# Kernel tuning notes

Measured on AMD Instinct MI355X. Metric: run time of the kernel, lower is better.

Reference implementation:

```python
import jax, jax.numpy as jnp
import numpy as np

EPS = 1e-12  # tf.math.l2_normalize epsilon

def _l2norm(x):
    # normalize over last axis, matching K.l2_normalize semantics
    sq = jnp.sum(x * x, axis=-1, keepdims=True)
    return x * jax.lax.rsqrt(jnp.maximum(sq, EPS))

def setup_inputs() -> dict:
    key = jax.random.key(0)
    k1, k2, k3 = jax.random.split(key, 3)
    B, L, D, P = 16, 256, 256, 20
    sent1 = jax.random.normal(k1, (B, L, D), dtype=jnp.float32)
    sent2 = jax.random.normal(k2, (B, L, D), dtype=jnp.float32)
    # glorot_uniform for shape (P, D)
    limit = np.sqrt(6.0 / (P + D)).astype(np.float32)
    kernel = jax.random.uniform(k3, (P, D), minval=-limit, maxval=limit, dtype=jnp.float32)
    return {"sent1": sent1, "sent2": sent2, "kernel": kernel}

def reference(sent1, sent2, kernel):
    # sent1: [B,L1,D], sent2: [B,L2,D], kernel: [P,D]
    v1 = _l2norm(sent1[:, :, None, :] * kernel)  # [B,L1,P,D]
    v2 = _l2norm(sent2[:, :, None, :] * kernel)  # [B,L2,P,D]
    # per-perspective cosine similarity matrix: [B,L1,L2,P]
    cos = jnp.einsum('blpd,bmpd->blmp', v1, v2)
    # max over the other sentence's positions (L2) -> [B,L1,P]
    return jnp.max(cos, axis=2)
```

## Files before the change

### kernel.cpp

```cpp
#include <hip/hip_runtime.h>
#include <hip/hip_bf16.h>


#define B_DIM 16
#define L_DIM 256
#define D_DIM 256
#define P_DIM 20
#define EPS 1e-12f
#define LDP 264

typedef __attribute__((ext_vector_type(8))) __bf16 bf16x8;
typedef __attribute__((ext_vector_type(4))) float f32x4;

__device__ __forceinline__ unsigned short f2bf(float x) {
  unsigned int u = __float_as_uint(x);
  u += 0x7fffu + ((u >> 16) & 1u);
  return (unsigned short)(u >> 16);
}

__global__ __launch_bounds__(256)
void prep2(const float* __restrict__ s1, const float* __restrict__ s2,
           const float* __restrict__ kg,
           float* __restrict__ rn1, float* __restrict__ rn2,
           unsigned short* __restrict__ s1bf, unsigned short* __restrict__ s2bf) {
  __shared__ __align__(16) unsigned short QA[32 * LDP];
  __shared__ __align__(16) unsigned short QB[32 * LDP];
  const int tid = threadIdx.x, lane = tid & 63, wave = tid >> 6;
  const int lr = lane & 15, q = lane >> 4;
  const int sent = blockIdx.x & 1, t = blockIdx.x >> 1;
  const int r0 = t * 32, b = r0 >> 8;
  const float* src = sent ? s2 : s1;
  unsigned short* sbf = sent ? s2bf : s1bf;
  float* rn = sent ? rn2 : rn1;

  #pragma unroll
  for (int i = 0; i < 8; ++i) {
    const int row = i * 4 + wave;
    float4 sv = *(const float4*)(src + (size_t)(r0 + row) * D_DIM + lane * 4);
    unsigned int c0 = ((unsigned int)f2bf(sv.y) << 16) | f2bf(sv.x);
    unsigned int c1 = ((unsigned int)f2bf(sv.w) << 16) | f2bf(sv.z);
    *(uint2*)&sbf[(size_t)(r0 + row) * D_DIM + lane * 4] = make_uint2(c0, c1);
    unsigned int q0 = ((unsigned int)f2bf(sv.y * sv.y) << 16) | f2bf(sv.x * sv.x);
    unsigned int q1 = ((unsigned int)f2bf(sv.w * sv.w) << 16) | f2bf(sv.z * sv.z);
    *(uint2*)&QA[row * LDP + lane * 4] = make_uint2(q0, q1);
  }
  #pragma unroll
  for (int j = 0; j < 5; ++j) {
    const int row = wave * 5 + j;
    float4 kv = *(const float4*)(kg + row * D_DIM + lane * 4);
    unsigned int c0 = ((unsigned int)f2bf(kv.y * kv.y) << 16) | f2bf(kv.x * kv.x);
    unsigned int c1 = ((unsigned int)f2bf(kv.w * kv.w) << 16) | f2bf(kv.z * kv.z);
    *(uint2*)&QB[row * LDP + lane * 4] = make_uint2(c0, c1);
  }
  __syncthreads();

  const int mt = wave & 1, nt = wave >> 1;
  f32x4 acc = {0.f, 0.f, 0.f, 0.f};
  #pragma unroll
  for (int ks = 0; ks < 8; ++ks) {
    const int cc = ks * 4 + q;
    bf16x8 a  = *(const bf16x8*)&QA[(mt * 16 + lr) * LDP + cc * 8];
    bf16x8 bb = *(const bf16x8*)&QB[(nt * 16 + lr) * LDP + cc * 8];
    acc = __builtin_amdgcn_mfma_f32_16x16x32_bf16(a, bb, acc, 0, 0, 0);
  }
  const int p = nt * 16 + lr;
  if (p < P_DIM) {
    #pragma unroll
    for (int r = 0; r < 4; ++r) {
      const int l = (r0 & 255) + mt * 16 + q * 4 + r;
      rn[((size_t)b * P_DIM + p) * L_DIM + l] = rsqrtf(fmaxf(acc[r], EPS));
    }
  }
}

__global__ __launch_bounds__(512, 4)
void mpm_main(const unsigned short* __restrict__ s1bf,
              const unsigned short* __restrict__ s2bf,
              const float* __restrict__ kg, const float* __restrict__ rn1,
              const float* __restrict__ rn2, float* __restrict__ outg) {
  __shared__ __align__(16) unsigned short X1[32 * 256];
  __shared__ float Wout[8 * 32];

  const int tid = threadIdx.x, lane = tid & 63, wave = tid >> 6;
  const int lr = lane & 15, q = lane >> 4;

  const int bid = (int)((blockIdx.x >> 3) + (blockIdx.x & 7) * 64);
  const int pgi = bid & 3, lt = (bid >> 2) & 7, b = bid >> 5;
  const int l0 = lt * 32;

  bf16x8 af[2][8];
  {
    const unsigned short* s2b2 = s2bf + (size_t)b * (L_DIM * D_DIM);
    #pragma unroll
    for (int mi = 0; mi < 2; ++mi) {
      const unsigned short* rp = s2b2 + (size_t)(wave * 32 + mi * 16 + lr) * D_DIM + q * 8;
      #pragma unroll
      for (int ks = 0; ks < 8; ++ks)
        af[mi][ks] = *(const bf16x8*)(rp + ks * 32);
    }
  }

  uint2 s1r[4];
  {
    const unsigned short* s1b2 = s1bf + ((size_t)b * L_DIM + l0) * D_DIM;
    #pragma unroll
    for (int i = 0; i < 4; ++i)
      s1r[i] = *(const uint2*)(s1b2 + (size_t)(i * 8 + wave) * D_DIM + lane * 4);
  }

  #pragma unroll 1
  for (int pp = 0; pp < 5; ++pp) {
    const int p = pgi * 5 + pp;

    {
      float4 kv = *(const float4*)(kg + (size_t)p * D_DIM + lane * 4);
      const float k0 = kv.x * kv.x, k1 = kv.y * kv.y, k2 = kv.z * kv.z, k3 = kv.w * kv.w;
      #pragma unroll
      for (int i = 0; i < 4; ++i) {
        const int row = i * 8 + wave;
        float x0 = __uint_as_float(s1r[i].x << 16)         * k0;
        float x1 = __uint_as_float(s1r[i].x & 0xffff0000u) * k1;
        float x2 = __uint_as_float(s1r[i].y << 16)         * k2;
        float x3 = __uint_as_float(s1r[i].y & 0xffff0000u) * k3;
        unsigned int c0 = ((unsigned int)f2bf(x1) << 16) | f2bf(x0);
        unsigned int c1 = ((unsigned int)f2bf(x3) << 16) | f2bf(x2);
        *(uint2*)&X1[row * 256 + (((lane >> 1) ^ row) << 3) + ((lane & 1) << 2)] =
            make_uint2(c0, c1);
      }
    }
    __syncthreads();

    f32x4 acc[2][2];
    #pragma unroll
    for (int mi = 0; mi < 2; ++mi)
      #pragma unroll
      for (int li = 0; li < 2; ++li) acc[mi][li] = (f32x4){0.f, 0.f, 0.f, 0.f};

    #pragma unroll
    for (int ks = 0; ks < 8; ++ks) {
      const int cc = ks * 4 + q;
      bf16x8 bb[2];
      #pragma unroll
      for (int li = 0; li < 2; ++li) {
        const int l = li * 16 + lr;
        bb[li] = *(const bf16x8*)&X1[l * 256 + ((cc ^ l) << 3)];
      }
      #pragma unroll
      for (int li = 0; li < 2; ++li) {
        acc[0][li] = __builtin_amdgcn_mfma_f32_16x16x32_bf16(af[0][ks], bb[li], acc[0][li], 0, 0, 0);
        acc[1][li] = __builtin_amdgcn_mfma_f32_16x16x32_bf16(af[1][ks], bb[li], acc[1][li], 0, 0, 0);
      }
    }

    float4 r20, r21;
    {
      const float* rn2b = rn2 + ((size_t)b * P_DIM + p) * L_DIM + wave * 32;
      r20 = *(const float4*)(rn2b + q * 4);
      r21 = *(const float4*)(rn2b + 16 + q * 4);
    }
    float v[2];
    #pragma unroll
    for (int li = 0; li < 2; ++li) {
      float t = -3.4e38f;
      t = fmaxf(t, fmaxf(acc[0][li][0] * r20.x, acc[1][li][0] * r21.x));
      t = fmaxf(t, fmaxf(acc[0][li][1] * r20.y, acc[1][li][1] * r21.y));
      t = fmaxf(t, fmaxf(acc[0][li][2] * r20.z, acc[1][li][2] * r21.z));
      t = fmaxf(t, fmaxf(acc[0][li][3] * r20.w, acc[1][li][3] * r21.w));
      t = fmaxf(t, __shfl_xor(t, 16));
      t = fmaxf(t, __shfl_xor(t, 32));
      v[li] = t;
    }
    if (q == 0) {
      #pragma unroll
      for (int li = 0; li < 2; ++li) Wout[wave * 32 + li * 16 + lr] = v[li];
    }
    __syncthreads();
    if (tid < 32) {
      float o = Wout[tid];
      #pragma unroll
      for (int w = 1; w < 8; ++w) o = fmaxf(o, Wout[w * 32 + tid]);
      const float r1 = rn1[((size_t)b * P_DIM + p) * L_DIM + l0 + tid];
      outg[((size_t)b * L_DIM + (l0 + tid)) * P_DIM + p] = o * r1;
    }
  }
}

extern "C" void kernel_launch(void* const* d_in, const int* in_sizes, int n_in,
                              void* d_out, int out_size, void* d_ws, size_t ws_size,
                              hipStream_t stream) {
  (void)in_sizes; (void)n_in; (void)out_size; (void)ws_size;
  const float* s1 = (const float*)d_in[0];
  const float* s2 = (const float*)d_in[1];
  const float* kg = (const float*)d_in[2];
  float* out = (float*)d_out;

  float* rn1 = (float*)d_ws;
  float* rn2 = rn1 + (size_t)B_DIM * P_DIM * L_DIM;
  unsigned short* s2bf = (unsigned short*)(rn2 + (size_t)B_DIM * P_DIM * L_DIM);
  unsigned short* s1bf = s2bf + (size_t)B_DIM * L_DIM * D_DIM;

  prep2<<<dim3(256), dim3(256), 0, stream>>>(s1, s2, kg, rn1, rn2, s1bf, s2bf);
  mpm_main<<<dim3(512), dim3(512), 0, stream>>>(s1bf, s2bf, kg, rn1, rn2, out);
}
```

Before: 88.89 us.

## Double-buffer scaled sent1 tiles and widen L1 tile to halve block count

Each block now covers 64 sentence-1 rows instead of 32, so the grid shrinks to 256 blocks and each sentence-2 fragment loaded into registers is reused across twice as many outputs. The scaled sent1 tile for the next perspective is built into a second LDS buffer while the MFMAs for the current one run, which removes one barrier per iteration. Kernel weights and rn1 values are hoisted out of the loop. The cost is higher register and LDS use per block (launch bounds lowered to 2) and fewer blocks to fill the 256 CUs.

```diff
diff --git a/kernel.cpp b/kernel.cpp
--- a/kernel.cpp
+++ b/kernel.cpp
@@ -73,20 +73,20 @@
   }
 }
 
-__global__ __launch_bounds__(512, 4)
+__global__ __launch_bounds__(512, 2)
 void mpm_main(const unsigned short* __restrict__ s1bf,
               const unsigned short* __restrict__ s2bf,
               const float* __restrict__ kg, const float* __restrict__ rn1,
               const float* __restrict__ rn2, float* __restrict__ outg) {
-  __shared__ __align__(16) unsigned short X1[32 * 256];
-  __shared__ float Wout[8 * 32];
+  __shared__ __align__(16) unsigned short X1[2][64 * 256];
+  __shared__ float Wout[2][8 * 64];
 
   const int tid = threadIdx.x, lane = tid & 63, wave = tid >> 6;
   const int lr = lane & 15, q = lane >> 4;
 
-  const int bid = (int)((blockIdx.x >> 3) + (blockIdx.x & 7) * 64);
-  const int pgi = bid & 3, lt = (bid >> 2) & 7, b = bid >> 5;
-  const int l0 = lt * 32;
+  const int bid = (int)((blockIdx.x >> 3) + (blockIdx.x & 7) * 32);
+  const int pgi = bid & 3, lt = (bid >> 2) & 3, b = bid >> 4;
+  const int l0 = lt * 64;
 
   bf16x8 af[2][8];
   {
@@ -100,67 +100,84 @@
     }
   }
 
-  uint2 s1r[4];
+  uint2 s1r[8];
   {
     const unsigned short* s1b2 = s1bf + ((size_t)b * L_DIM + l0) * D_DIM;
     #pragma unroll
-    for (int i = 0; i < 4; ++i)
+    for (int i = 0; i < 8; ++i)
       s1r[i] = *(const uint2*)(s1b2 + (size_t)(i * 8 + wave) * D_DIM + lane * 4);
   }
 
+  float4 kv2[5];
+  #pragma unroll
+  for (int j = 0; j < 5; ++j) {
+    float4 t = *(const float4*)(kg + (size_t)(pgi * 5 + j) * D_DIM + lane * 4);
+    kv2[j] = make_float4(t.x * t.x, t.y * t.y, t.z * t.z, t.w * t.w);
+  }
+
+  float rn1v[5];
+  if (tid < 64) {
+    #pragma unroll
+    for (int j = 0; j < 5; ++j)
+      rn1v[j] = rn1[((size_t)b * P_DIM + pgi * 5 + j) * L_DIM + l0 + tid];
+  }
+
+  auto build = [&](unsigned short* dst, int j) {
+    const float4 kv = kv2[j];
+    #pragma unroll
+    for (int i = 0; i < 8; ++i) {
+      const int row = i * 8 + wave;
+      float x0 = __uint_as_float(s1r[i].x << 16)         * kv.x;
+      float x1 = __uint_as_float(s1r[i].x & 0xffff0000u) * kv.y;
+      float x2 = __uint_as_float(s1r[i].y << 16)         * kv.z;
+      float x3 = __uint_as_float(s1r[i].y & 0xffff0000u) * kv.w;
+      unsigned int c0 = ((unsigned int)f2bf(x1) << 16) | f2bf(x0);
+      unsigned int c1 = ((unsigned int)f2bf(x3) << 16) | f2bf(x2);
+      *(uint2*)&dst[row * 256 + (((lane >> 1) ^ (row & 31)) << 3) + ((lane & 1) << 2)] =
+          make_uint2(c0, c1);
+    }
+  };
+
+  build(X1[0], 0);
+  __syncthreads();
+
+  int par = 0;
   #pragma unroll 1
   for (int pp = 0; pp < 5; ++pp) {
     const int p = pgi * 5 + pp;
 
-    {
-      float4 kv = *(const float4*)(kg + (size_t)p * D_DIM + lane * 4);
-      const float k0 = kv.x * kv.x, k1 = kv.y * kv.y, k2 = kv.z * kv.z, k3 = kv.w * kv.w;
-      #pragma unroll
-      for (int i = 0; i < 4; ++i) {
-        const int row = i * 8 + wave;
-        float x0 = __uint_as_float(s1r[i].x << 16)         * k0;
-        float x1 = __uint_as_float(s1r[i].x & 0xffff0000u) * k1;
-        float x2 = __uint_as_float(s1r[i].y << 16)         * k2;
-        float x3 = __uint_as_float(s1r[i].y & 0xffff0000u) * k3;
-        unsigned int c0 = ((unsigned int)f2bf(x1) << 16) | f2bf(x0);
-        unsigned int c1 = ((unsigned int)f2bf(x3) << 16) | f2bf(x2);
-        *(uint2*)&X1[row * 256 + (((lane >> 1) ^ row) << 3) + ((lane & 1) << 2)] =
-            make_uint2(c0, c1);
-      }
-    }
-    __syncthreads();
-
-    f32x4 acc[2][2];
+    const float* rn2b = rn2 + ((size_t)b * P_DIM + p) * L_DIM + wave * 32;
+    float4 r20 = *(const float4*)(rn2b + q * 4);
+    float4 r21 = *(const float4*)(rn2b + 16 + q * 4);
+
+    if (pp < 4) build(X1[par ^ 1], pp + 1);
+
+    f32x4 acc[2][4];
     #pragma unroll
     for (int mi = 0; mi < 2; ++mi)
       #pragma unroll
-      for (int li = 0; li < 2; ++li) acc[mi][li] = (f32x4){0.f, 0.f, 0.f, 0.f};
-
+      for (int li = 0; li < 4; ++li) acc[mi][li] = (f32x4){0.f, 0.f, 0.f, 0.f};
+
+    const unsigned short* Xc = X1[par];
     #pragma unroll
     for (int ks = 0; ks < 8; ++ks) {
       const int cc = ks * 4 + q;
-      bf16x8 bb[2];
-      #pragma unroll
-      for (int li = 0; li < 2; ++li) {
+      bf16x8 bb[4];
+      #pragma unroll
+      for (int li = 0; li < 4; ++li) {
         const int l = li * 16 + lr;
-        bb[li] = *(const bf16x8*)&X1[l * 256 + ((cc ^ l) << 3)];
+        bb[li] = *(const bf16x8*)&Xc[l * 256 + ((cc ^ (l & 31)) << 3)];
       }
       #pragma unroll
-      for (int li = 0; li < 2; ++li) {
+      for (int li = 0; li < 4; ++li) {
         acc[0][li] = __builtin_amdgcn_mfma_f32_16x16x32_bf16(af[0][ks], bb[li], acc[0][li], 0, 0, 0);
         acc[1][li] = __builtin_amdgcn_mfma_f32_16x16x32_bf16(af[1][ks], bb[li], acc[1][li], 0, 0, 0);
       }
     }
 
-    float4 r20, r21;
-    {
-      const float* rn2b = rn2 + ((size_t)b * P_DIM + p) * L_DIM + wave * 32;
-      r20 = *(const float4*)(rn2b + q * 4);
-      r21 = *(const float4*)(rn2b + 16 + q * 4);
-    }
-    float v[2];
-    #pragma unroll
-    for (int li = 0; li < 2; ++li) {
+    float v[4];
+    #pragma unroll
+    for (int li = 0; li < 4; ++li) {
       float t = -3.4e38f;
       t = fmaxf(t, fmaxf(acc[0][li][0] * r20.x, acc[1][li][0] * r21.x));
       t = fmaxf(t, fmaxf(acc[0][li][1] * r20.y, acc[1][li][1] * r21.y));
@@ -172,16 +189,16 @@
     }
     if (q == 0) {
       #pragma unroll
-      for (int li = 0; li < 2; ++li) Wout[wave * 32 + li * 16 + lr] = v[li];
+      for (int li = 0; li < 4; ++li) Wout[par][wave * 64 + li * 16 + lr] = v[li];
     }
     __syncthreads();
-    if (tid < 32) {
-      float o = Wout[tid];
-      #pragma unroll
-      for (int w = 1; w < 8; ++w) o = fmaxf(o, Wout[w * 32 + tid]);
-      const float r1 = rn1[((size_t)b * P_DIM + p) * L_DIM + l0 + tid];
-      outg[((size_t)b * L_DIM + (l0 + tid)) * P_DIM + p] = o * r1;
-    }
+    if (tid < 64) {
+      float o = Wout[par][tid];
+      #pragma unroll
+      for (int w = 1; w < 8; ++w) o = fmaxf(o, Wout[par][w * 64 + tid]);
+      outg[((size_t)b * L_DIM + (l0 + tid)) * P_DIM + p] = o * rn1v[pp];
+    }
+    par ^= 1;
   }
 }
 
@@ -200,5 +217,5 @@
   unsigned short* s1bf = s2bf + (size_t)B_DIM * L_DIM * D_DIM;
 
   prep2<<<dim3(256), dim3(256), 0, stream>>>(s1, s2, kg, rn1, rn2, s1bf, s2bf);
-  mpm_main<<<dim3(512), dim3(512), 0, stream>>>(s1bf, s2bf, kg, rn1, rn2, out);
-}
+  mpm_main<<<dim3(256), dim3(512), 0, stream>>>(s1bf, s2bf, kg, rn1, rn2, out);
+}
```

After: 82.30 us. -7.4%, faster.
